# Optimization experiments

Measured on AMD Instinct MI355X. Metric: run time of the kernel, lower is better.

## Reference

```python
import jax, jax.numpy as jnp
import numpy as np

IN_F, OUT_F, RANK = 4096, 4096, 1024
B, S_LEN = 4, 2048


def _dequant(data, scale, zp):
    # (int_data - zero_point) * scale, per-tensor scalar quantization
    return (data.astype(jnp.float32) - zp.astype(jnp.float32)) * scale.astype(jnp.float32)


def setup_inputs() -> dict:
    key = jax.random.key(0)
    ks = jax.random.split(key, 8)
    x = jax.random.normal(ks[0], (B, S_LEN, IN_F), dtype=jnp.float32)
    U_data = jax.random.randint(ks[1], (OUT_F, RANK), 0, 255, dtype=jnp.int32)
    S_data = jax.random.randint(ks[2], (RANK,), 0, 255, dtype=jnp.int32)
    Vh_data = jax.random.randint(ks[3], (RANK, IN_F), 0, 255, dtype=jnp.int32)
    bias = jax.random.normal(ks[4], (OUT_F,), dtype=jnp.float32)
    return {
        "x": x,
        "U_data": U_data,
        "U_scale": jnp.array([0.02], dtype=jnp.float32),
        "U_zp": jnp.array([128.0], dtype=jnp.float32),
        "S_data": S_data,
        "S_scale": jnp.array([0.05], dtype=jnp.float32),
        "S_zp": jnp.array([128.0], dtype=jnp.float32),
        "Vh_data": Vh_data,
        "Vh_scale": jnp.array([0.02], dtype=jnp.float32),
        "Vh_zp": jnp.array([128.0], dtype=jnp.float32),
        "bias": bias,
    }


def reference(x, U_data, U_scale, U_zp, S_data, S_scale, S_zp,
              Vh_data, Vh_scale, Vh_zp, bias):
    U = _dequant(U_data, U_scale, U_zp)     # [out, r]
    S = _dequant(S_data, S_scale, S_zp)     # [r]
    Vh = _dequant(Vh_data, Vh_scale, Vh_zp)  # [r, in]
    orig_shape = x.shape
    x_flat = x.reshape(-1, orig_shape[-1])  # [N, in]
    h = x_flat @ Vh.T                        # [N, r]
    h = h * S[None, :]
    y = h @ U.T                              # [N, out]
    y = y + bias
    return y.reshape(orig_shape[:-1] + (U.shape[0],))
```

## Files before the change

### kernel.cpp

```cpp
#include <hip/hip_runtime.h>
#include <stdint.h>

#define NROWS 8192
#define INF   4096
#define OUTF  4096
#define RNK   1024

typedef unsigned short u16;
typedef __attribute__((ext_vector_type(8))) short bf16x8;
typedef __attribute__((ext_vector_type(4))) float f32x4;
typedef __attribute__((ext_vector_type(8))) unsigned short u16x8;

__device__ __forceinline__ u16 f32_bf16(float f) {
  union { float f; uint32_t u; } v; v.f = f;
  return (u16)((v.u + 0x7FFF + ((v.u >> 16) & 1)) >> 16);
}


__global__ __launch_bounds__(256) void convert_x(const float* __restrict__ x,
                                                 u16* __restrict__ o) {
  int t = blockIdx.x * 256 + threadIdx.x;
  int e = t * 8;
  float4 a = *(const float4*)(x + e);
  float4 b = *(const float4*)(x + e + 4);
  u16x8 r;
  r[0] = f32_bf16(a.x); r[1] = f32_bf16(a.y); r[2] = f32_bf16(a.z); r[3] = f32_bf16(a.w);
  r[4] = f32_bf16(b.x); r[5] = f32_bf16(b.y); r[6] = f32_bf16(b.z); r[7] = f32_bf16(b.w);
  *(u16x8*)(o + e) = r;
}

__global__ __launch_bounds__(256) void dequant_vh(const int* __restrict__ vh,
                                                  const float* __restrict__ vs,
                                                  const float* __restrict__ vz,
                                                  const int* __restrict__ sd,
                                                  const float* __restrict__ ss,
                                                  const float* __restrict__ sz,
                                                  u16* __restrict__ o) {
  int t = blockIdx.x * 256 + threadIdx.x;
  int e = t * 4;
  int row = e >> 12;
  float sval = ((float)sd[row] - sz[0]) * ss[0];
  float sc = vs[0] * sval;
  float zp = vz[0];
  int4 d = *(const int4*)(vh + e);
  ushort4 r;
  r.x = f32_bf16(((float)d.x - zp) * sc);
  r.y = f32_bf16(((float)d.y - zp) * sc);
  r.z = f32_bf16(((float)d.z - zp) * sc);
  r.w = f32_bf16(((float)d.w - zp) * sc);
  *(ushort4*)(o + e) = r;
}

__global__ __launch_bounds__(256) void dequant_u(const int* __restrict__ ud,
                                                 const float* __restrict__ us,
                                                 const float* __restrict__ uz,
                                                 u16* __restrict__ o) {
  int t = blockIdx.x * 256 + threadIdx.x;
  int e = t * 4;
  float sc = us[0];
  float zp = uz[0];
  int4 d = *(const int4*)(ud + e);
  ushort4 r;
  r.x = f32_bf16(((float)d.x - zp) * sc);
  r.y = f32_bf16(((float)d.y - zp) * sc);
  r.z = f32_bf16(((float)d.z - zp) * sc);
  r.w = f32_bf16(((float)d.w - zp) * sc);
  *(ushort4*)(o + e) = r;
}


__device__ __forceinline__ void gl_lds16(const u16* g, u16* l) {
  __builtin_amdgcn_global_load_lds(
      (const __attribute__((address_space(1))) void*)g,
      (__attribute__((address_space(3))) void*)l, 16, 0, 0);
}

template <int VM> __device__ __forceinline__ void vm_wait() {
  static_assert(VM == 3 || VM == 4, "unexpected vmcnt");
  if constexpr (VM == 3) asm volatile("s_waitcnt vmcnt(3)" ::: "memory");
  if constexpr (VM == 4) asm volatile("s_waitcnt vmcnt(4)" ::: "memory");
}

template <int BN, int WM, int WN, int K, int N, bool OUT_BF16, bool ADD_BIAS>
__global__ __launch_bounds__(512, 2) void gemm4p(const u16* __restrict__ A,
                                                 const u16* __restrict__ B,
                                                 void* __restrict__ Cv,
                                                 const float* __restrict__ bias) {
  constexpr int BM = 256, BK = 64;
  constexpr int AR = 128 / WM;
  constexpr int BC = (BN / 2) / WN;
  constexpr int AI = AR / 16;
  constexpr int BJ = BC / 16;
  constexpr int LB = (BN == 256) ? 2 : 1;
  constexpr int NT = K / BK;
  constexpr int AH = 128 * BK;
  constexpr int BH = (BN / 2) * BK;

  __shared__ __attribute__((aligned(16))) u16 ldsA[2 * 2 * AH];
  __shared__ __attribute__((aligned(16))) u16 ldsB[2 * 2 * BH];

  const int tid  = threadIdx.x;
  const int lane = tid & 63;
  const int wave = tid >> 6;
  const int wn   = wave % WN;
  const int wm   = wave / WN;
  const int bm   = blockIdx.y * BM;
  const int bn   = blockIdx.x * BN;

  const int srow = tid >> 3;
  const int spc  = tid & 7;
  const int sgc  = spc ^ (srow & 7);

  const u16* gA = A + (size_t)(bm + srow) * K + sgc * 8;
  const u16* gB = B + (size_t)(bn + srow) * K + sgc * 8;
  u16* lA = ldsA + srow * BK + spc * 8;
  u16* lB = ldsB + srow * BK + spc * 8;

#define STAGE_A(buf, h, kt)                                                    \
  { const u16* g_ = gA + (size_t)(h) * 128 * K + (kt);                         \
    u16* l_ = lA + ((buf) * 2 + (h)) * AH;                                     \
    gl_lds16(g_, l_);                                                          \
    gl_lds16(g_ + (size_t)64 * K, l_ + 64 * BK); }

#define STAGE_B(buf, h, kt)                                                    \
  { const u16* g_ = gB + (size_t)(h) * (BN / 2) * K + (kt);                    \
    u16* l_ = lB + ((buf) * 2 + (h)) * BH;                                     \
    gl_lds16(g_, l_);                                                          \
    if constexpr (LB == 2) gl_lds16(g_ + (size_t)64 * K, l_ + 64 * BK); }

  const int r   = lane & 15;
  const int kq  = (lane >> 4) * 8;
  const int pc0 = (((kq) >> 3) ^ (r & 7)) << 3;
  const int pc1 = (((32 + kq) >> 3) ^ (r & 7)) << 3;

  f32x4 acc[2][2][AI][BJ] = {};
  bf16x8 af[AI][2];
  bf16x8 bf0[BJ][2];
  bf16x8 bf1[BJ][2];

#define LOAD_A(buf, ih)                                                        \
  { const u16* ab = ldsA + ((buf) * 2 + (ih)) * AH + (wm * AR + r) * BK;       \
    _Pragma("unroll")                                                          \
    for (int i = 0; i < AI; ++i) {                                             \
      af[i][0] = *(const bf16x8*)(ab + i * 16 * BK + pc0);                     \
      af[i][1] = *(const bf16x8*)(ab + i * 16 * BK + pc1);                     \
    } }

#define LOAD_B(dst, buf, jh)                                                   \
  { const u16* bb = ldsB + ((buf) * 2 + (jh)) * BH + (wn * BC + r) * BK;       \
    _Pragma("unroll")                                                          \
    for (int j = 0; j < BJ; ++j) {                                             \
      dst[j][0] = *(const bf16x8*)(bb + j * 16 * BK + pc0);                    \
      dst[j][1] = *(const bf16x8*)(bb + j * 16 * BK + pc1);                    \
    } }

#define MFMA_Q(ih, jh, bsrc)                                                   \
  _Pragma("unroll")                                                            \
  for (int i = 0; i < AI; ++i)                                                 \
    _Pragma("unroll")                                                          \
    for (int j = 0; j < BJ; ++j) {                                             \
      acc[ih][jh][i][j] = __builtin_amdgcn_mfma_f32_16x16x32_bf16(             \
          af[i][0], bsrc[j][0], acc[ih][jh][i][j], 0, 0, 0);                   \
      acc[ih][jh][i][j] = __builtin_amdgcn_mfma_f32_16x16x32_bf16(             \
          af[i][1], bsrc[j][1], acc[ih][jh][i][j], 0, 0, 0);                   \
    }

#define SB  __builtin_amdgcn_sched_barrier(0)
#define BAR __builtin_amdgcn_s_barrier()
#define PRIO1 __builtin_amdgcn_s_setprio(1)
#define PRIO0 __builtin_amdgcn_s_setprio(0)

  STAGE_A(0, 0, 0);
  STAGE_B(0, 0, 0);
  STAGE_B(0, 1, 0);
  STAGE_A(0, 1, 0);
  SB;
  constexpr int KT1 = (NT > 1 ? BK : 0);
  STAGE_A(1, 0, KT1);
  STAGE_B(1, 1, KT1);
  SB;
  vm_wait<2 + LB>();
  BAR;
  SB;

  for (int t = 0; t < NT; ++t) {
    const int buf  = t & 1;
    const int nbuf = buf ^ 1;
    const int kt1 = (t + 1 < NT ? t + 1 : NT - 1) * BK;
    const int kt2 = (t + 2 < NT ? t + 2 : NT - 1) * BK;

    LOAD_A(buf, 0); LOAD_B(bf0, buf, 0);
    STAGE_A(nbuf, 1, kt1);
    SB; BAR; SB; PRIO1;
    MFMA_Q(0, 0, bf0);
    PRIO0; SB; BAR; SB;

    LOAD_B(bf1, buf, 1);
    STAGE_B(nbuf, 0, kt1);
    SB; BAR; SB; PRIO1;
    MFMA_Q(0, 1, bf1);
    PRIO0; SB; BAR; SB;

    LOAD_A(buf, 1);
    STAGE_A(buf, 0, kt2);
    SB; BAR; SB; PRIO1;
    MFMA_Q(1, 1, bf1);
    PRIO0; SB; BAR; SB;

    STAGE_B(buf, 1, kt2);
    SB; BAR; SB; PRIO1;
    MFMA_Q(1, 0, bf0);
    PRIO0; SB;
    vm_wait<2 + LB>();
    BAR; SB;
  }

  const int col0 = lane & 15;
  const int row0 = (lane >> 4) * 4;
#pragma unroll
  for (int ih = 0; ih < 2; ++ih)
#pragma unroll
    for (int jh = 0; jh < 2; ++jh)
#pragma unroll
      for (int j = 0; j < BJ; ++j) {
        const int gcol = bn + jh * (BN / 2) + wn * BC + j * 16 + col0;
        float bv = 0.f;
        if constexpr (ADD_BIAS) bv = bias[gcol];
#pragma unroll
        for (int i = 0; i < AI; ++i)
#pragma unroll
          for (int rr = 0; rr < 4; ++rr) {
            const int grow = bm + ih * 128 + wm * AR + i * 16 + row0 + rr;
            float v = acc[ih][jh][i][j][rr] + bv;
            if constexpr (OUT_BF16)
              ((u16*)Cv)[(size_t)grow * N + gcol] = f32_bf16(v);
            else
              ((float*)Cv)[(size_t)grow * N + gcol] = v;
          }
      }
#undef MFMA_Q
#undef LOAD_A
#undef LOAD_B
#undef STAGE_A
#undef STAGE_B
#undef SB
#undef BAR
#undef PRIO1
#undef PRIO0
}


extern "C" void kernel_launch(void* const* d_in, const int* in_sizes, int n_in,
                              void* d_out, int out_size, void* d_ws, size_t ws_size,
                              hipStream_t stream) {
  const float* x        = (const float*)d_in[0];
  const int*   U_data   = (const int*)d_in[1];
  const float* U_scale  = (const float*)d_in[2];
  const float* U_zp     = (const float*)d_in[3];
  const int*   S_data   = (const int*)d_in[4];
  const float* S_scale  = (const float*)d_in[5];
  const float* S_zp     = (const float*)d_in[6];
  const int*   Vh_data  = (const int*)d_in[7];
  const float* Vh_scale = (const float*)d_in[8];
  const float* Vh_zp    = (const float*)d_in[9];
  const float* bias     = (const float*)d_in[10];
  float* out = (float*)d_out;

  char* ws = (char*)d_ws;
  u16* xb  = (u16*)ws;
  u16* vhb = (u16*)(ws + (size_t)67108864);
  u16* ub  = (u16*)(ws + (size_t)67108864 + 8388608);
  u16* hb  = (u16*)(ws + (size_t)67108864 + 16777216);

  convert_x<<<NROWS * INF / (8 * 256), 256, 0, stream>>>(x, xb);
  dequant_vh<<<RNK * INF / (4 * 256), 256, 0, stream>>>(Vh_data, Vh_scale, Vh_zp,
                                                        S_data, S_scale, S_zp, vhb);
  dequant_u<<<OUTF * RNK / (4 * 256), 256, 0, stream>>>(U_data, U_scale, U_zp, ub);

  gemm4p<128, 4, 2, INF, RNK, true, false>
      <<<dim3(RNK / 128, NROWS / 256), 512, 0, stream>>>(xb, vhb, (void*)hb, nullptr);

  gemm4p<256, 2, 4, RNK, OUTF, false, true>
      <<<dim3(OUTF / 256, NROWS / 256), 512, 0, stream>>>(hb, ub, (void*)out, bias);
}
```

Measured before the change: 447.8 us.

## Add triple-buffered LDS pipeline to first GEMM and XCD-aware block swizzle

The first GEMM (x·Vhᵀ) gains a three-buffer LDS pipeline that prefetches two K-tiles ahead with a single vmcnt(6) wait per iteration. Both GEMMs remap workgroup ids so tiles assigned to the same XCD are contiguous, aiming at better L2 locality. The extra buffer raises the first GEMM's LDS use to about 144 KB, which limits it to one block per CU.

```diff
diff --git a/kernel.cpp b/kernel.cpp
--- a/kernel.cpp
+++ b/kernel.cpp
@@ -76,12 +76,13 @@
 }
 
 template <int VM> __device__ __forceinline__ void vm_wait() {
-  static_assert(VM == 3 || VM == 4, "unexpected vmcnt");
+  static_assert(VM == 3 || VM == 4 || VM == 6, "unexpected vmcnt");
   if constexpr (VM == 3) asm volatile("s_waitcnt vmcnt(3)" ::: "memory");
   if constexpr (VM == 4) asm volatile("s_waitcnt vmcnt(4)" ::: "memory");
-}
-
-template <int BN, int WM, int WN, int K, int N, bool OUT_BF16, bool ADD_BIAS>
+  if constexpr (VM == 6) asm volatile("s_waitcnt vmcnt(6)" ::: "memory");
+}
+
+template <int BN, int WM, int WN, int K, int N, int NBUF, bool OUT_BF16, bool ADD_BIAS>
 __global__ __launch_bounds__(512, 2) void gemm4p(const u16* __restrict__ A,
                                                  const u16* __restrict__ B,
                                                  void* __restrict__ Cv,
@@ -96,16 +97,25 @@
   constexpr int AH = 128 * BK;
   constexpr int BH = (BN / 2) * BK;
 
-  __shared__ __attribute__((aligned(16))) u16 ldsA[2 * 2 * AH];
-  __shared__ __attribute__((aligned(16))) u16 ldsB[2 * 2 * BH];
+  constexpr int NXB = N / BN;
+  constexpr int NYB = NROWS / BM;
+  constexpr int NWG = NXB * NYB;
+  static_assert(NWG % 8 == 0, "XCD swizzle requires nwg % 8 == 0");
+  constexpr int CPX = NWG / 8;
+
+  __shared__ __attribute__((aligned(16))) u16 ldsA[NBUF * 2 * AH];
+  __shared__ __attribute__((aligned(16))) u16 ldsB[NBUF * 2 * BH];
 
   const int tid  = threadIdx.x;
   const int lane = tid & 63;
   const int wave = tid >> 6;
   const int wn   = wave % WN;
   const int wm   = wave / WN;
-  const int bm   = blockIdx.y * BM;
-  const int bn   = blockIdx.x * BN;
+
+  const int L    = blockIdx.y * NXB + blockIdx.x;
+  const int orig = (L & 7) * CPX + (L >> 3);
+  const int bm   = (orig / NXB) * BM;
+  const int bn   = (orig % NXB) * BN;
 
   const int srow = tid >> 3;
   const int spc  = tid & 7;
@@ -170,49 +180,90 @@
 #define PRIO1 __builtin_amdgcn_s_setprio(1)
 #define PRIO0 __builtin_amdgcn_s_setprio(0)
 
-  STAGE_A(0, 0, 0);
-  STAGE_B(0, 0, 0);
-  STAGE_B(0, 1, 0);
-  STAGE_A(0, 1, 0);
-  SB;
-  constexpr int KT1 = (NT > 1 ? BK : 0);
-  STAGE_A(1, 0, KT1);
-  STAGE_B(1, 1, KT1);
-  SB;
-  vm_wait<2 + LB>();
-  BAR;
-  SB;
-
-  for (int t = 0; t < NT; ++t) {
-    const int buf  = t & 1;
-    const int nbuf = buf ^ 1;
-    const int kt1 = (t + 1 < NT ? t + 1 : NT - 1) * BK;
-    const int kt2 = (t + 2 < NT ? t + 2 : NT - 1) * BK;
-
-    LOAD_A(buf, 0); LOAD_B(bf0, buf, 0);
-    STAGE_A(nbuf, 1, kt1);
-    SB; BAR; SB; PRIO1;
-    MFMA_Q(0, 0, bf0);
-    PRIO0; SB; BAR; SB;
-
-    LOAD_B(bf1, buf, 1);
-    STAGE_B(nbuf, 0, kt1);
-    SB; BAR; SB; PRIO1;
-    MFMA_Q(0, 1, bf1);
-    PRIO0; SB; BAR; SB;
-
-    LOAD_A(buf, 1);
-    STAGE_A(buf, 0, kt2);
-    SB; BAR; SB; PRIO1;
-    MFMA_Q(1, 1, bf1);
-    PRIO0; SB; BAR; SB;
-
-    STAGE_B(buf, 1, kt2);
-    SB; BAR; SB; PRIO1;
-    MFMA_Q(1, 0, bf0);
-    PRIO0; SB;
+  if constexpr (NBUF == 3) {
+    static_assert(LB == 1, "NBUF==3 path sized for BN==128");
+    STAGE_A(0, 0, 0); STAGE_B(0, 0, 0); STAGE_A(0, 1, 0); STAGE_B(0, 1, 0);
+    constexpr int KT1 = (NT > 1 ? BK : 0);
+    STAGE_A(1, 0, KT1); STAGE_B(1, 0, KT1); STAGE_A(1, 1, KT1); STAGE_B(1, 1, KT1);
+    SB;
+    vm_wait<6>();
+    BAR; SB;
+
+    int buf = 0, bufn = 1, sbuf = 2;
+    for (int t = 0; t < NT; ++t) {
+      const int kt2 = (t + 2 < NT ? t + 2 : NT - 1) * BK;
+
+      LOAD_A(buf, 0); LOAD_B(bf0, buf, 0);
+      STAGE_A(sbuf, 0, kt2);
+      SB; BAR; SB; PRIO1;
+      MFMA_Q(0, 0, bf0);
+      PRIO0; SB; BAR; SB;
+
+      LOAD_B(bf1, buf, 1);
+      STAGE_B(sbuf, 0, kt2);
+      SB; BAR; SB; PRIO1;
+      MFMA_Q(0, 1, bf1);
+      PRIO0; SB; BAR; SB;
+
+      LOAD_A(buf, 1);
+      STAGE_A(sbuf, 1, kt2);
+      SB; BAR; SB; PRIO1;
+      MFMA_Q(1, 1, bf1);
+      PRIO0; SB; BAR; SB;
+
+      STAGE_B(sbuf, 1, kt2);
+      SB; BAR; SB; PRIO1;
+      MFMA_Q(1, 0, bf0);
+      PRIO0; SB;
+      vm_wait<6>();
+      BAR; SB;
+
+      const int tmp = buf; buf = bufn; bufn = sbuf; sbuf = tmp;
+    }
+  } else {
+    STAGE_A(0, 0, 0);
+    STAGE_B(0, 0, 0);
+    STAGE_B(0, 1, 0);
+    STAGE_A(0, 1, 0);
+    SB;
+    constexpr int KT1 = (NT > 1 ? BK : 0);
+    STAGE_A(1, 0, KT1);
+    STAGE_B(1, 1, KT1);
+    SB;
     vm_wait<2 + LB>();
     BAR; SB;
+
+    for (int t = 0; t < NT; ++t) {
+      const int buf  = t & 1;
+      const int nbuf = buf ^ 1;
+      const int kt1 = (t + 1 < NT ? t + 1 : NT - 1) * BK;
+      const int kt2 = (t + 2 < NT ? t + 2 : NT - 1) * BK;
+
+      LOAD_A(buf, 0); LOAD_B(bf0, buf, 0);
+      STAGE_A(nbuf, 1, kt1);
+      SB; BAR; SB; PRIO1;
+      MFMA_Q(0, 0, bf0);
+      PRIO0; SB; BAR; SB;
+
+      LOAD_B(bf1, buf, 1);
+      STAGE_B(nbuf, 0, kt1);
+      SB; BAR; SB; PRIO1;
+      MFMA_Q(0, 1, bf1);
+      PRIO0; SB; BAR; SB;
+
+      LOAD_A(buf, 1);
+      STAGE_A(buf, 0, kt2);
+      SB; BAR; SB; PRIO1;
+      MFMA_Q(1, 1, bf1);
+      PRIO0; SB; BAR; SB;
+
+      STAGE_B(buf, 1, kt2);
+      SB; BAR; SB; PRIO1;
+      MFMA_Q(1, 0, bf0);
+      PRIO0; SB;
+      vm_wait<2 + LB>();
+      BAR; SB;
+    }
   }
 
   const int col0 = lane & 15;
@@ -277,9 +328,9 @@
                                                         S_data, S_scale, S_zp, vhb);
   dequant_u<<<OUTF * RNK / (4 * 256), 256, 0, stream>>>(U_data, U_scale, U_zp, ub);
 
-  gemm4p<128, 4, 2, INF, RNK, true, false>
+  gemm4p<128, 4, 2, INF, RNK, 3, true, false>
       <<<dim3(RNK / 128, NROWS / 256), 512, 0, stream>>>(xb, vhb, (void*)hb, nullptr);
 
-  gemm4p<256, 2, 4, RNK, OUTF, false, true>
+  gemm4p<256, 2, 4, RNK, OUTF, 2, false, true>
       <<<dim3(OUTF / 256, NROWS / 256), 512, 0, stream>>>(hb, ub, (void*)out, bias);
 }
```

New measurement: 418.0 us. 1.07x faster.

## Merge GEMM main loop into two barrier phases and add XCD-aware block swizzle

Applied to the files above, without the earlier changes.

The per-iteration schedule of the GEMM kernel is reduced from four barrier-separated quarter phases to two, with each phase issuing two MFMA quarters after grouping its LDS reads and global-to-LDS stages. Separately, workgroup indices are remapped so that consecutive tiles land on the same XCD, improving L2 locality across the chiplets. Fewer barriers should cut synchronisation stalls. The cost is more register pressure from holding both B fragments at once, and a risk of LDS hazards because the stage into the current buffer now sits closer to the reads of that buffer.

```diff
diff --git a/kernel.cpp b/kernel.cpp
--- a/kernel.cpp
+++ b/kernel.cpp
@@ -82,7 +82,7 @@
 }
 
 template <int BN, int WM, int WN, int K, int N, bool OUT_BF16, bool ADD_BIAS>
-__global__ __launch_bounds__(512, 2) void gemm4p(const u16* __restrict__ A,
+__global__ __launch_bounds__(512, 2) void gemm2b(const u16* __restrict__ A,
                                                  const u16* __restrict__ B,
                                                  void* __restrict__ Cv,
                                                  const float* __restrict__ bias) {
@@ -96,6 +96,12 @@
   constexpr int AH = 128 * BK;
   constexpr int BH = (BN / 2) * BK;
 
+  constexpr int NXB = N / BN;
+  constexpr int NYB = NROWS / BM;
+  constexpr int NWG = NXB * NYB;
+  static_assert(NWG % 8 == 0, "XCD swizzle requires nwg % 8 == 0");
+  constexpr int CPX = NWG / 8;
+
   __shared__ __attribute__((aligned(16))) u16 ldsA[2 * 2 * AH];
   __shared__ __attribute__((aligned(16))) u16 ldsB[2 * 2 * BH];
 
@@ -104,8 +110,11 @@
   const int wave = tid >> 6;
   const int wn   = wave % WN;
   const int wm   = wave / WN;
-  const int bm   = blockIdx.y * BM;
-  const int bn   = blockIdx.x * BN;
+
+  const int L    = blockIdx.y * NXB + blockIdx.x;
+  const int orig = (L & 7) * CPX + (L >> 3);
+  const int bm   = (orig / NXB) * BM;
+  const int bn   = (orig % NXB) * BN;
 
   const int srow = tid >> 3;
   const int spc  = tid & 7;
@@ -180,8 +189,7 @@
   STAGE_B(1, 1, KT1);
   SB;
   vm_wait<2 + LB>();
-  BAR;
-  SB;
+  BAR; SB;
 
   for (int t = 0; t < NT; ++t) {
     const int buf  = t & 1;
@@ -189,28 +197,23 @@
     const int kt1 = (t + 1 < NT ? t + 1 : NT - 1) * BK;
     const int kt2 = (t + 2 < NT ? t + 2 : NT - 1) * BK;
 
-    LOAD_A(buf, 0); LOAD_B(bf0, buf, 0);
+    LOAD_A(buf, 0);
+    LOAD_B(bf0, buf, 0);
+    LOAD_B(bf1, buf, 1);
     STAGE_A(nbuf, 1, kt1);
-    SB; BAR; SB; PRIO1;
-    MFMA_Q(0, 0, bf0);
-    PRIO0; SB; BAR; SB;
-
-    LOAD_B(bf1, buf, 1);
     STAGE_B(nbuf, 0, kt1);
-    SB; BAR; SB; PRIO1;
-    MFMA_Q(0, 1, bf1);
-    PRIO0; SB; BAR; SB;
-
+    SB;
+    PRIO1; MFMA_Q(0, 0, bf0); PRIO0;
+    PRIO1; MFMA_Q(0, 1, bf1); PRIO0;
+    SB; BAR; SB;
+
+    STAGE_A(buf, 0, kt2);
+    STAGE_B(buf, 1, kt2);
+    SB;
     LOAD_A(buf, 1);
-    STAGE_A(buf, 0, kt2);
-    SB; BAR; SB; PRIO1;
-    MFMA_Q(1, 1, bf1);
-    PRIO0; SB; BAR; SB;
-
-    STAGE_B(buf, 1, kt2);
-    SB; BAR; SB; PRIO1;
-    MFMA_Q(1, 0, bf0);
-    PRIO0; SB;
+    PRIO1; MFMA_Q(1, 1, bf1); PRIO0;
+    PRIO1; MFMA_Q(1, 0, bf0); PRIO0;
+    SB;
     vm_wait<2 + LB>();
     BAR; SB;
   }
@@ -277,9 +280,9 @@
                                                         S_data, S_scale, S_zp, vhb);
   dequant_u<<<OUTF * RNK / (4 * 256), 256, 0, stream>>>(U_data, U_scale, U_zp, ub);
 
-  gemm4p<128, 4, 2, INF, RNK, true, false>
+  gemm2b<128, 4, 2, INF, RNK, true, false>
       <<<dim3(RNK / 128, NROWS / 256), 512, 0, stream>>>(xb, vhb, (void*)hb, nullptr);
 
-  gemm4p<256, 2, 4, RNK, OUTF, false, true>
+  gemm2b<256, 2, 4, RNK, OUTF, false, true>
       <<<dim3(OUTF / 256, NROWS / 256), 512, 0, stream>>>(hb, ub, (void*)out, bias);
 }
```

After: 420.9 us. -6.0%, faster.
